# Kernel optimization log

Measured on AMD Instinct MI355X. Metric: run time of the kernel, lower is better.

## Reference

```python
import jax, jax.numpy as jnp
import numpy as np

B, S, D, H = 4, 2048, 1024, 16
DH = D // H
LN_EPS = 1e-5


def setup_inputs() -> dict:
    key = jax.random.key(0)
    ks = jax.random.split(key, 8)
    q = jax.random.normal(ks[0], (B, S, D), dtype=jnp.float32)
    k = jax.random.normal(ks[1], (B, S, D), dtype=jnp.float32)
    v = jax.random.normal(ks[2], (B, S, D), dtype=jnp.float32)
    masks = jax.random.randint(ks[3], (B, S, S), 0, 2, dtype=jnp.int32)
    proj_Q = jax.random.normal(ks[4], (D,), dtype=jnp.float32)
    proj_K = jax.random.normal(ks[5], (D,), dtype=jnp.float32)
    proj_V = jax.random.normal(ks[6], (D,), dtype=jnp.float32)
    gamma = jnp.ones((D,), dtype=jnp.float32)
    beta = jnp.zeros((D,), dtype=jnp.float32)
    return {"q": q, "k": k, "v": v, "masks": masks,
            "proj_Q": proj_Q, "proj_K": proj_K, "proj_V": proj_V,
            "gamma": gamma, "beta": beta}


def _split_heads(x):
    # x: [B,S,D] -> permute(0,2,1) -> [B,D,S] -> view(B*H, DH, S) -> permute -> [B*H, S, DH]
    xt = jnp.transpose(x, (0, 2, 1))              # [B,D,S]
    xt = xt.reshape(B * H, DH, S)                 # [B*H,DH,S] (batch-major head split)
    return jnp.transpose(xt, (0, 2, 1))           # [B*H,S,DH]


def reference(q, k, v, masks, proj_Q, proj_K, proj_V, gamma, beta):
    # Source bug preserved: projections all applied to `x` == q; k, v are ignored.
    x = q
    Qh = _split_heads(x * proj_Q)                 # [B*H,S,DH]
    Kh = _split_heads(x * proj_K)
    Vh = _split_heads(x * proj_V)

    # masks cat'd along dim 0 num_head times (head-major tiling, as in source)
    m = jnp.tile(masks, (H, 1, 1)).astype(bool)   # [H*B,S,S]

    scores = jnp.einsum('nqd,nkd->nqk', Qh, Kh) / jnp.sqrt(jnp.float32(D))
    scores = jnp.where(m, jnp.float32(-1e-10), scores)  # source uses -1e-10, not -inf
    attn = jax.nn.softmax(scores, axis=2)
    ctx = jnp.einsum('nqk,nkd->nqd', attn, Vh)    # [B*H,S,DH]

    # merge heads back: [B*H,S,DH] -> [B*H,DH,S] -> [B,D,S] -> [B,S,D]
    ctx = jnp.transpose(ctx, (0, 2, 1)).reshape(B, D, S)
    ctx = jnp.transpose(ctx, (0, 2, 1))

    out = ctx + q                                  # dropout(p=0) is identity
    mu = jnp.mean(out, axis=-1, keepdims=True)
    var = jnp.var(out, axis=-1, keepdims=True)
    out = (out - mu) * jax.lax.rsqrt(var + LN_EPS) * gamma + beta
    return out
```

## Files before the change

### kernel.cpp

```cpp
#include <hip/hip_runtime.h>
#include <math.h>

#define Bn 4
#define Sn 2048
#define Dn 1024
#define Hn 16
#define DHn 64
#define QT 128
#define KT 64
#define STR 72

typedef __attribute__((ext_vector_type(8))) short short8;
typedef __attribute__((ext_vector_type(4))) float f32x4;

__device__ __forceinline__ ushort f2bf(float f) {
    union { float f; unsigned u; } x; x.f = f;
    unsigned r = x.u + 0x7fffu + ((x.u >> 16) & 1u);
    return (ushort)(r >> 16);
}

__device__ __forceinline__ unsigned pack_bf2(float lo, float hi) {
    unsigned r;
    asm("v_cvt_pk_bf16_f32 %0, %1, %2" : "=v"(r) : "v"(lo), "v"(hi));
    return r;
}

__device__ __forceinline__ float fexp2(float x) { return __builtin_amdgcn_exp2f(x); }

__global__ __launch_bounds__(256)
void prep_kv3(const float* __restrict__ xin, const float* __restrict__ pK,
              const float* __restrict__ pV, ushort* __restrict__ Kw,
              ushort* __restrict__ Vw)
{
    __shared__ ushort LK[64 * STR];
    __shared__ ushort LV[64 * STR];
    const int kt = blockIdx.x, n = blockIdx.y, b = n >> 4, h = n & 15;
    const int t = threadIdx.x;
    const int sl = t >> 2, dq = (t & 3) * 16;

    const float* xp  = xin + ((size_t)b * Sn + kt * 64 + sl) * Dn + h * DHn + dq;
    const float* pkp = pK + h * DHn + dq;
    const float* pvp = pV + h * DHn + dq;

    float xv[16], pk[16], pv[16];
    #pragma unroll
    for (int j = 0; j < 4; ++j) {
        float4 a  = ((const float4*)xp)[j];
        float4 kk = ((const float4*)pkp)[j];
        float4 vv = ((const float4*)pvp)[j];
        xv[4*j+0] = a.x;  xv[4*j+1] = a.y;  xv[4*j+2] = a.z;  xv[4*j+3] = a.w;
        pk[4*j+0] = kk.x; pk[4*j+1] = kk.y; pk[4*j+2] = kk.z; pk[4*j+3] = kk.w;
        pv[4*j+0] = vv.x; pv[4*j+1] = vv.y; pv[4*j+2] = vv.z; pv[4*j+3] = vv.w;
    }
    unsigned kw[8], vw[8];
    #pragma unroll
    for (int j = 0; j < 8; ++j) {
        kw[j] = pack_bf2(xv[2*j] * pk[2*j], xv[2*j+1] * pk[2*j+1]);
        vw[j] = pack_bf2(xv[2*j] * pv[2*j], xv[2*j+1] * pv[2*j+1]);
    }
    *(uint4*)&LK[sl * STR + dq]     = make_uint4(kw[0], kw[1], kw[2], kw[3]);
    *(uint4*)&LK[sl * STR + dq + 8] = make_uint4(kw[4], kw[5], kw[6], kw[7]);
    *(uint4*)&LV[sl * STR + dq]     = make_uint4(vw[0], vw[1], vw[2], vw[3]);
    *(uint4*)&LV[sl * STR + dq + 8] = make_uint4(vw[4], vw[5], vw[6], vw[7]);
    __syncthreads();

    ushort* kout = Kw + ((size_t)n * 32 + kt) * 4096;
    ushort* vout = Vw + ((size_t)n * 32 + kt) * 4096;
    #pragma unroll
    for (int i = 0; i < 2; ++i) {
        int c  = t * 2 + i;
        int f  = c >> 6, lc = c & 63;
        int key = (f >> 1) * 16 + (lc & 15);
        int dh0 = (f & 1) * 32 + (lc >> 4) * 8;
        *(uint4*)(kout + c * 8) = *(const uint4*)&LK[key * STR + dh0];
        int dg = f & 3, hh = f >> 2;
        int dhv = dg * 16 + (lc & 15);
        ushort tmp[8];
        #pragma unroll
        for (int e = 0; e < 8; ++e) {
            int p  = hh * 32 + (lc >> 4) * 8 + e;
            int ss = (p & 32) | ((p & 4) << 2) | ((p & 24) >> 1) | (p & 3);
            tmp[e] = LV[ss * STR + dhv];
        }
        unsigned o0 = (unsigned)tmp[0] | ((unsigned)tmp[1] << 16);
        unsigned o1 = (unsigned)tmp[2] | ((unsigned)tmp[3] << 16);
        unsigned o2 = (unsigned)tmp[4] | ((unsigned)tmp[5] << 16);
        unsigned o3 = (unsigned)tmp[6] | ((unsigned)tmp[7] << 16);
        *(uint4*)(vout + c * 8) = make_uint4(o0, o1, o2, o3);
    }
}

__global__ __launch_bounds__(256)
void mask_pack(const int* __restrict__ masks, unsigned long long* __restrict__ mpack)
{
    const int t = threadIdx.x, l = t & 63;
    const int wid_g = (blockIdx.x * 256 + t) >> 6;
    #pragma unroll 4
    for (int i = 0; i < 16; ++i) {
        int word = wid_g * 16 + i;
        int row  = word >> 5, wd = word & 31;
        int m = masks[(size_t)row * 2048 + wd * 64 + l];
        unsigned long long bits = __ballot(m != 0);
        if (l == 0) mpack[word] = bits;
    }
}

__global__ __launch_bounds__(256, 2)
void attn_fast3(const float* __restrict__ xin, const unsigned long long* __restrict__ mpack,
                const float* __restrict__ pQ, const ushort* __restrict__ Kw,
                const ushort* __restrict__ Vw, float* __restrict__ out)
{
    __shared__ __attribute__((aligned(16))) ushort S[16384];

    const int id   = blockIdx.x;
    const int xcd  = id & 7, pos = id >> 3;
    const int n    = (pos >> 4) * 8 + xcd;
    const int q0   = (pos & 15) * 128;
    const int b    = n >> 4;
    const int h    = n & 15;
    const int mb   = n & 3;

    const int t  = threadIdx.x;
    const int w  = t >> 6;
    const int l  = t & 63;
    const int G  = l >> 4;
    const int li = l & 15;
    const int G4 = G * 4;

    const float C2 = 0.0450842200277800f;
    const float* xb = xin + (size_t)b * Sn * Dn + h * DHn;
    const float pq_s = pQ[h * DHn + l] * C2;
    #pragma unroll
    for (int i = 0; i < 8; ++i) {
        #pragma unroll
        for (int j = 0; j < 4; ++j) {
            int qr = i * 4 + j;
            float v = xb[(size_t)(q0 + w * 32 + qr) * Dn + l];
            S[(w * 32 + qr) * STR + l] = f2bf(v * pq_s);
        }
    }
    short8 qf[2][2];
    #pragma unroll
    for (int qs = 0; qs < 2; ++qs)
        #pragma unroll
        for (int kk = 0; kk < 2; ++kk)
            qf[qs][kk] = *(const short8*)&S[(w*32 + qs*16 + li) * STR + kk*32 + G*8];
    __syncthreads();

    const f32x4 Z4 = {0.f, 0.f, 0.f, 0.f};
    const short8 VONES = {(short)0x3F80, (short)0x3F80, (short)0x3F80, (short)0x3F80,
                          (short)0x3F80, (short)0x3F80, (short)0x3F80, (short)0x3F80};

    f32x4 acc_o[2][4];
    f32x4 acc_l[2];
    #pragma unroll
    for (int qs = 0; qs < 2; ++qs) {
        #pragma unroll
        for (int dg = 0; dg < 4; ++dg) acc_o[qs][dg] = (f32x4){0.f, 0.f, 0.f, 0.f};
        acc_l[qs] = (f32x4){0.f, 0.f, 0.f, 0.f};
    }

    const ushort* kwf = Kw + (size_t)n * 131072 + (w * 2) * 512 + (size_t)l * 8;
    const ushort* vwf = Vw + (size_t)n * 131072 + (w * 2) * 512 + (size_t)l * 8;
    const int fo0 = (w * 2) * 512 + l * 8;
    const int fo1 = (w * 2 + 1) * 512 + l * 8;

    const int row0 = q0 + w * 32 + li;
    const unsigned long long* mrow0 = mpack + (size_t)(mb * 2048 + row0) * 32;
    const unsigned long long* mrow1 = mpack + (size_t)(mb * 2048 + row0 + 16) * 32;

    unsigned long long mA0, mA1, mB0, mB1;

    {
        short8 a = *(const short8*)kwf;
        short8 c = *(const short8*)(kwf + 512);
        short8 d = *(const short8*)vwf;
        short8 e = *(const short8*)(vwf + 512);
        mA0 = mrow0[0]; mA1 = mrow1[0];
        *(short8*)&S[fo0] = a;
        *(short8*)&S[fo1] = c;
        *(short8*)&S[8192 + fo0] = d;
        *(short8*)&S[8192 + fo1] = e;
    }

#define BODY(CUR, NXT, MC0, MC1, MN0, MN1, KTv, PF)                                   \
    {                                                                                  \
        __syncthreads();                     \
               \
        f32x4 s_[2][4];                                                                \
        __builtin_amdgcn_s_setprio(1);                                                 \
        _Pragma("unroll")                                                              \
        for (int kg = 0; kg < 4; ++kg) {                                               \
            short8 kf0 = *(const short8*)&S[(CUR)*4096 + (kg*2+0)*512 + l*8];          \
            short8 kf1 = *(const short8*)&S[(CUR)*4096 + (kg*2+1)*512 + l*8];          \
            s_[0][kg] = __builtin_amdgcn_mfma_f32_16x16x32_bf16(kf0, qf[0][0], Z4, 0, 0, 0); \
            s_[1][kg] = __builtin_amdgcn_mfma_f32_16x16x32_bf16(kf0, qf[1][0], Z4, 0, 0, 0); \
            s_[0][kg] = __builtin_amdgcn_mfma_f32_16x16x32_bf16(kf1, qf[0][1], s_[0][kg], 0, 0, 0); \
            s_[1][kg] = __builtin_amdgcn_mfma_f32_16x16x32_bf16(kf1, qf[1][1], s_[1][kg], 0, 0, 0); \
        }                                                                              \
        __builtin_amdgcn_s_setprio(0);                                                 \
                        \
        short8 kst0, kst1, vst0, vst1;                                                 \
        if (PF) {                                                                      \
            const ushort* kp = kwf + (size_t)((KTv)+1) * 4096;                         \
            const ushort* vp = vwf + (size_t)((KTv)+1) * 4096;                         \
            kst0 = *(const short8*)kp;  kst1 = *(const short8*)(kp + 512);             \
            vst0 = *(const short8*)vp;  vst1 = *(const short8*)(vp + 512);             \
            MN0 = mrow0[(KTv)+1];       MN1 = mrow1[(KTv)+1];                          \
        }                                                                              \
                         \
        short8 pf[2][2];                                                               \
        _Pragma("unroll")                                                              \
        for (int qs = 0; qs < 2; ++qs) {                                               \
            unsigned mlo = (unsigned)(qs ? (MC1) : (MC0));                             \
            unsigned mhi = (unsigned)((qs ? (MC1) : (MC0)) >> 32);                     \
            float ev[16];                                                              \
            _Pragma("unroll")                                                          \
            for (int kg = 0; kg < 4; ++kg) {                                           \
                unsigned dw  = (kg < 2) ? mlo : mhi;                                   \
                unsigned nib = (dw >> ((kg & 1) * 16 + G4)) & 15u;                     \
                _Pragma("unroll")                                                      \
                for (int r = 0; r < 4; ++r) {                                          \
                    float tt = (nib & (1u << r)) ? 0.f : s_[qs][kg][r];                \
                    ev[kg*4 + r] = fexp2(tt);                                          \
                }                                                                      \
            }                                                                          \
            _Pragma("unroll")                                                          \
            for (int hh = 0; hh < 2; ++hh) {                                           \
                union { unsigned u[4]; short8 v; } pu;                                 \
                pu.u[0] = pack_bf2(ev[hh*8+0], ev[hh*8+1]);                            \
                pu.u[1] = pack_bf2(ev[hh*8+2], ev[hh*8+3]);                            \
                pu.u[2] = pack_bf2(ev[hh*8+4], ev[hh*8+5]);                            \
                pu.u[3] = pack_bf2(ev[hh*8+6], ev[hh*8+7]);                            \
                pf[qs][hh] = pu.v;                                                     \
            }                                                                          \
        }                                                                              \
                                                \
        __builtin_amdgcn_s_setprio(1);                                                 \
        _Pragma("unroll")                                                              \
        for (int hh = 0; hh < 2; ++hh) {                                               \
            short8 vf0 = *(const short8*)&S[8192 + (CUR)*4096 + (hh*4+0)*512 + l*8];   \
            short8 vf1 = *(const short8*)&S[8192 + (CUR)*4096 + (hh*4+1)*512 + l*8];   \
            short8 vf2 = *(const short8*)&S[8192 + (CUR)*4096 + (hh*4+2)*512 + l*8];   \
            short8 vf3 = *(const short8*)&S[8192 + (CUR)*4096 + (hh*4+3)*512 + l*8];   \
            _Pragma("unroll")                                                          \
            for (int qs = 0; qs < 2; ++qs) {                                           \
                acc_o[qs][0] = __builtin_amdgcn_mfma_f32_16x16x32_bf16(pf[qs][hh], vf0, acc_o[qs][0], 0, 0, 0); \
                acc_o[qs][1] = __builtin_amdgcn_mfma_f32_16x16x32_bf16(pf[qs][hh], vf1, acc_o[qs][1], 0, 0, 0); \
                acc_o[qs][2] = __builtin_amdgcn_mfma_f32_16x16x32_bf16(pf[qs][hh], vf2, acc_o[qs][2], 0, 0, 0); \
                acc_o[qs][3] = __builtin_amdgcn_mfma_f32_16x16x32_bf16(pf[qs][hh], vf3, acc_o[qs][3], 0, 0, 0); \
                acc_l[qs]    = __builtin_amdgcn_mfma_f32_16x16x32_bf16(pf[qs][hh], VONES, acc_l[qs], 0, 0, 0); \
            }                                                                          \
        }                                                                              \
        __builtin_amdgcn_s_setprio(0);                                                 \
        \
        if (PF) {                                                                      \
            *(short8*)&S[(NXT)*4096 + fo0] = kst0;                                     \
            *(short8*)&S[(NXT)*4096 + fo1] = kst1;                                     \
            *(short8*)&S[8192 + (NXT)*4096 + fo0] = vst0;                              \
            *(short8*)&S[8192 + (NXT)*4096 + fo1] = vst1;                              \
        }                                                                              \
    }

    for (int kt = 0; kt < 32; kt += 2) {
        BODY(0, 1, mA0, mA1, mB0, mB1, kt, true)
        BODY(1, 0, mB0, mB1, mA0, mA1, kt + 1, (kt + 1 < 31))
    }
#undef BODY

    #pragma unroll
    for (int qs = 0; qs < 2; ++qs) {
        #pragma unroll
        for (int r = 0; r < 4; ++r) {
            float inv = 1.f / acc_l[qs][r];
            int qg = q0 + w*32 + qs*16 + G4 + r;
            float* ob = out + ((size_t)b * Sn + qg) * Dn + h * DHn;
            #pragma unroll
            for (int dg = 0; dg < 4; ++dg)
                ob[dg*16 + li] = acc_o[qs][dg][r] * inv;
        }
    }
}

__global__ __launch_bounds__(256)
void prep_kv(const float* __restrict__ xin, const float* __restrict__ pK,
             const float* __restrict__ pV, ushort* __restrict__ Kbf,
             ushort* __restrict__ Vtw)
{
    __shared__ ushort Ls[64 * STR];
    const int n = blockIdx.y, b = n >> 4, h = n & 15;
    const int s0 = blockIdx.x * 64;
    const int t = threadIdx.x;
    const int sl = t >> 2, dq = (t & 3) * 16;

    const float* xp = xin + (size_t)b * Sn * Dn + (size_t)(s0 + sl) * Dn + h * DHn + dq;
    const float* pkp = pK + h * DHn + dq;
    const float* pvp = pV + h * DHn + dq;

    float xv[16], pk[16], pv[16];
    #pragma unroll
    for (int j = 0; j < 4; ++j) {
        float4 a = ((const float4*)xp)[j];
        float4 kk = ((const float4*)pkp)[j];
        float4 vv = ((const float4*)pvp)[j];
        xv[4*j+0] = a.x;  xv[4*j+1] = a.y;  xv[4*j+2] = a.z;  xv[4*j+3] = a.w;
        pk[4*j+0] = kk.x; pk[4*j+1] = kk.y; pk[4*j+2] = kk.z; pk[4*j+3] = kk.w;
        pv[4*j+0] = vv.x; pv[4*j+1] = vv.y; pv[4*j+2] = vv.z; pv[4*j+3] = vv.w;
    }
    unsigned kw[8], vw[8];
    #pragma unroll
    for (int j = 0; j < 8; ++j) {
        kw[j] = pack_bf2(xv[2*j] * pk[2*j], xv[2*j+1] * pk[2*j+1]);
        vw[j] = pack_bf2(xv[2*j] * pv[2*j], xv[2*j+1] * pv[2*j+1]);
    }
    ushort* kdst = Kbf + ((size_t)n * Sn + s0 + sl) * DHn + dq;
    *(uint4*)kdst       = make_uint4(kw[0], kw[1], kw[2], kw[3]);
    *(uint4*)(kdst + 8) = make_uint4(kw[4], kw[5], kw[6], kw[7]);

    *(uint4*)&Ls[sl * STR + dq]     = make_uint4(vw[0], vw[1], vw[2], vw[3]);
    *(uint4*)&Ls[sl * STR + dq + 8] = make_uint4(vw[4], vw[5], vw[6], vw[7]);
    __syncthreads();

    const int dh = t >> 2, p4 = t & 3;
    ushort ov[16];
    #pragma unroll
    for (int j = 0; j < 16; ++j) {
        int p  = p4 * 16 + j;
        int ss = (p & 32) | ((p & 4) << 2) | ((p & 24) >> 1) | (p & 3);
        ov[j] = Ls[ss * STR + dh];
    }
    unsigned ow[8];
    #pragma unroll
    for (int j = 0; j < 8; ++j) ow[j] = (unsigned)ov[2*j] | ((unsigned)ov[2*j+1] << 16);
    ushort* vdst = Vtw + ((size_t)n * DHn + dh) * Sn + s0 + p4 * 16;
    *(uint4*)vdst       = make_uint4(ow[0], ow[1], ow[2], ow[3]);
    *(uint4*)(vdst + 8) = make_uint4(ow[4], ow[5], ow[6], ow[7]);
}

__global__ __launch_bounds__(256, 4)
void attn_fast2(const float* __restrict__ xin, const int* __restrict__ masks,
                const float* __restrict__ pQ, const ushort* __restrict__ Kbf,
                const ushort* __restrict__ Vtw, float* __restrict__ out)
{
    __shared__ ushort Ks[KT * STR];
    __shared__ ushort Vts[DHn * STR];

    const int n  = blockIdx.y;
    const int b  = n >> 4;
    const int h  = n & 15;
    const int mb = n & 3;
    const int q0 = blockIdx.x * QT;

    const int t  = threadIdx.x;
    const int w  = t >> 6;
    const int l  = t & 63;
    const int G  = l >> 4;
    const int li = l & 15;

    const float C2 = 0.0450842200277800f;
    const float* xb = xin + (size_t)b * Sn * Dn + h * DHn;
    const float pq_s = pQ[h * DHn + l] * C2;
    ushort* qstage = ((w < 2) ? Ks : Vts) + (w & 1) * (32 * STR);
    #pragma unroll
    for (int i = 0; i < 8; ++i) {
        #pragma unroll
        for (int j = 0; j < 4; ++j) {
            int qr = i * 4 + j;
            float v = xb[(size_t)(q0 + w * 32 + qr) * Dn + l];
            qstage[qr * STR + l] = f2bf(v * pq_s);
        }
    }
    short8 qf[2][2];
    #pragma unroll
    for (int qs = 0; qs < 2; ++qs)
        #pragma unroll
        for (int kk = 0; kk < 2; ++kk)
            qf[qs][kk] = *(const short8*)&qstage[(qs*16 + li) * STR + kk*32 + G*8];

    f32x4 acc_o[2][4];
    float lsum[2];
    #pragma unroll
    for (int qs = 0; qs < 2; ++qs) {
        #pragma unroll
        for (int dg = 0; dg < 4; ++dg) acc_o[qs][dg] = (f32x4){0.f, 0.f, 0.f, 0.f};
        lsum[qs] = 0.f;
    }

    const int* mq = masks + (size_t)mb * Sn * Sn + (size_t)(q0 + w*32 + li) * Sn;

    const int srow = w * 16 + (l >> 2);
    const int part = (l & 3) * 16;
    const ushort* ksrc = Kbf + (size_t)n * Sn * DHn + (size_t)srow * DHn + part;
    const ushort* vsrc = Vtw + (size_t)n * DHn * Sn + (size_t)srow * Sn + part;
    ushort* kdst = &Ks[srow * STR + part];
    ushort* vdst = &Vts[srow * STR + part];

    for (int kt = 0; kt < Sn / KT; ++kt) {
        __syncthreads();
        const ushort* kp = ksrc + (size_t)kt * KT * DHn;
        const ushort* vp = vsrc + kt * KT;
        short8 k0 = *(const short8*)kp, k1 = *(const short8*)(kp + 8);
        short8 v0 = *(const short8*)vp, v1 = *(const short8*)(vp + 8);
        *(short8*)kdst       = k0;
        *(short8*)(kdst + 8) = k1;
        *(short8*)vdst       = v0;
        *(short8*)(vdst + 8) = v1;
        __syncthreads();

        f32x4 s[2][4];
        #pragma unroll
        for (int qs = 0; qs < 2; ++qs)
            #pragma unroll
            for (int kg = 0; kg < 4; ++kg) s[qs][kg] = (f32x4){0.f, 0.f, 0.f, 0.f};
        __builtin_amdgcn_s_setprio(1);
        #pragma unroll
        for (int kg = 0; kg < 4; ++kg) {
            #pragma unroll
            for (int kk = 0; kk < 2; ++kk) {
                short8 kf = *(const short8*)&Ks[(kg*16 + li) * STR + kk*32 + G*8];
                s[0][kg] = __builtin_amdgcn_mfma_f32_16x16x32_bf16(kf, qf[0][kk], s[0][kg], 0, 0, 0);
                s[1][kg] = __builtin_amdgcn_mfma_f32_16x16x32_bf16(kf, qf[1][kk], s[1][kg], 0, 0, 0);
            }
        }
        __builtin_amdgcn_s_setprio(0);

        short8 pf[2][2];
        #pragma unroll
        for (int qs = 0; qs < 2; ++qs) {
            int4 mv[4];
            #pragma unroll
            for (int kg = 0; kg < 4; ++kg)
                mv[kg] = *(const int4*)(mq + (size_t)qs*16*Sn + kt*KT + kg*16 + G*4);
            float ev[16];
            #pragma unroll
            for (int kg = 0; kg < 4; ++kg) {
                int ma[4] = {mv[kg].x, mv[kg].y, mv[kg].z, mv[kg].w};
                #pragma unroll
                for (int r = 0; r < 4; ++r) {
                    float tt = ma[r] ? 0.f : s[qs][kg][r];
                    ev[kg*4 + r] = fexp2(tt);
                }
            }
            lsum[qs] += (((ev[0]+ev[1])+(ev[2]+ev[3])) + ((ev[4]+ev[5])+(ev[6]+ev[7])))
                      + (((ev[8]+ev[9])+(ev[10]+ev[11])) + ((ev[12]+ev[13])+(ev[14]+ev[15])));
            #pragma unroll
            for (int hh = 0; hh < 2; ++hh) {
                union { unsigned u[4]; short8 v; } pu;
                pu.u[0] = pack_bf2(ev[hh*8+0], ev[hh*8+1]);
                pu.u[1] = pack_bf2(ev[hh*8+2], ev[hh*8+3]);
                pu.u[2] = pack_bf2(ev[hh*8+4], ev[hh*8+5]);
                pu.u[3] = pack_bf2(ev[hh*8+6], ev[hh*8+7]);
                pf[qs][hh] = pu.v;
            }
        }

        #pragma unroll
        for (int hh = 0; hh < 2; ++hh) {
            short8 vf[4];
            #pragma unroll
            for (int dg = 0; dg < 4; ++dg)
                vf[dg] = *(const short8*)&Vts[(dg*16 + li) * STR + hh*32 + G*8];
            __builtin_amdgcn_s_setprio(1);
            #pragma unroll
            for (int qs = 0; qs < 2; ++qs)
                #pragma unroll
                for (int dg = 0; dg < 4; ++dg)
                    acc_o[qs][dg] = __builtin_amdgcn_mfma_f32_16x16x32_bf16(pf[qs][hh], vf[dg], acc_o[qs][dg], 0, 0, 0);
            __builtin_amdgcn_s_setprio(0);
        }
    }

    #pragma unroll
    for (int qs = 0; qs < 2; ++qs) {
        float v = lsum[qs];
        v += __shfl_xor(v, 16, 64);
        v += __shfl_xor(v, 32, 64);
        lsum[qs] = v;
    }

    #pragma unroll
    for (int qs = 0; qs < 2; ++qs) {
        #pragma unroll
        for (int r = 0; r < 4; ++r) {
            float lv = __shfl(lsum[qs], (l & 48) | (G * 4 + r), 64);
            float inv = 1.f / lv;
            int qg = q0 + w*32 + qs*16 + G*4 + r;
            float* ob = out + ((size_t)b * Sn + qg) * Dn + h * DHn;
            #pragma unroll
            for (int dg = 0; dg < 4; ++dg)
                ob[dg*16 + li] = acc_o[qs][dg][r] * inv;
        }
    }
}

__global__ __launch_bounds__(256)
void ln_kernel(const float* __restrict__ qin, const float* __restrict__ gamma,
               const float* __restrict__ beta, float* __restrict__ out)
{
    const int row = blockIdx.x;
    const int t   = threadIdx.x;
    const size_t base = (size_t)row * Dn + t * 4;

    float4 c = *(const float4*)(out + base);
    float4 r = *(const float4*)(qin + base);
    float4 v = make_float4(c.x + r.x, c.y + r.y, c.z + r.z, c.w + r.w);

    float sum = v.x + v.y + v.z + v.w;
    float sq  = v.x * v.x + v.y * v.y + v.z * v.z + v.w * v.w;
    #pragma unroll
    for (int off = 32; off >= 1; off >>= 1) {
        sum += __shfl_xor(sum, off, 64);
        sq  += __shfl_xor(sq,  off, 64);
    }
    __shared__ float as_[4], aq_[4];
    const int wid = t >> 6, ln = t & 63;
    if (ln == 0) { as_[wid] = sum; aq_[wid] = sq; }
    __syncthreads();
    sum = as_[0] + as_[1] + as_[2] + as_[3];
    sq  = aq_[0] + aq_[1] + aq_[2] + aq_[3];

    const float mean = sum * (1.f / Dn);
    const float var  = sq * (1.f / Dn) - mean * mean;
    const float rstd = rsqrtf(var + 1e-5f);

    float4 ga = *(const float4*)(gamma + t * 4);
    float4 be = *(const float4*)(beta + t * 4);
    float4 o;
    o.x = (v.x - mean) * rstd * ga.x + be.x;
    o.y = (v.y - mean) * rstd * ga.y + be.y;
    o.z = (v.z - mean) * rstd * ga.z + be.z;
    o.w = (v.w - mean) * rstd * ga.w + be.w;
    *(float4*)(out + base) = o;
}

extern "C" void kernel_launch(void* const* d_in, const int* in_sizes, int n_in,
                              void* d_out, int out_size, void* d_ws, size_t ws_size,
                              hipStream_t stream) {
    const float* q     = (const float*)d_in[0];
    const int*   masks = (const int*)d_in[3];
    const float* pQ    = (const float*)d_in[4];
    const float* pK    = (const float*)d_in[5];
    const float* pV    = (const float*)d_in[6];
    const float* gamma = (const float*)d_in[7];
    const float* beta  = (const float*)d_in[8];
    float* out = (float*)d_out;
    (void)in_sizes; (void)n_in; (void)out_size;

    const size_t elems = (size_t)Bn * Hn * Sn * DHn;
    const size_t kvbytes = elems * 2 * sizeof(ushort);
    const size_t need3 = kvbytes + (size_t)4 * Sn * 32 * 8;

    if (ws_size >= need3) {
        ushort* Kw = (ushort*)d_ws;
        ushort* Vw = Kw + elems;
        unsigned long long* mpack = (unsigned long long*)((char*)d_ws + kvbytes);
        prep_kv3<<<dim3(32, 64), 256, 0, stream>>>(q, pK, pV, Kw, Vw);
        mask_pack<<<4096, 256, 0, stream>>>(masks, mpack);
        attn_fast3<<<1024, 256, 0, stream>>>(q, mpack, pQ, Kw, Vw, out);
    } else if (ws_size >= kvbytes) {
        ushort* Kbf = (ushort*)d_ws;
        ushort* Vtw = Kbf + elems;
        prep_kv<<<dim3(Sn / 64, Bn * Hn), 256, 0, stream>>>(q, pK, pV, Kbf, Vtw);
        attn_fast2<<<dim3(Sn / QT, Bn * Hn), 256, 0, stream>>>(q, masks, pQ, Kbf, Vtw, out);
    }
    ln_kernel<<<Bn * Sn, 256, 0, stream>>>(q, gamma, beta, out);
}
```

Baseline: 140.4 us.

## Fuse KV prep with mask packing, tighten mask select asm, raise occupancy hint

The K/V prep kernel and the mask bit-packing kernel are merged into one launch, with blocks past 2048 doing mask packing, which removes a kernel launch and lets the two memory-bound phases overlap. Inside the attention loop, the nibble extraction and masked-score select are rewritten with v_bfe/v_bfi inline asm instead of compiler-generated shifts and selects. The attention kernel's launch bounds go from 2 to 3 blocks per CU, which caps registers and may cause spills.

New measurement: 137.9 us. About the same (-1.8%).

```diff
diff --git a/kernel.cpp b/kernel.cpp
--- a/kernel.cpp
+++ b/kernel.cpp
@@ -27,15 +27,38 @@
 
 __device__ __forceinline__ float fexp2(float x) { return __builtin_amdgcn_exp2f(x); }
 
+__device__ __forceinline__ float mask_sel(unsigned nib, int r, float s) {
+    int sx; unsigned tb;
+    asm("v_bfe_i32 %0, %1, %2, 1" : "=v"(sx) : "v"(nib), "i"(r));
+    asm("v_bfi_b32 %0, %1, 0, %2" : "=v"(tb) : "v"(sx), "v"(__float_as_uint(s)));
+    return __uint_as_float(tb);
+}
+
 __global__ __launch_bounds__(256)
-void prep_kv3(const float* __restrict__ xin, const float* __restrict__ pK,
-              const float* __restrict__ pV, ushort* __restrict__ Kw,
-              ushort* __restrict__ Vw)
+void prep_fused(const float* __restrict__ xin, const float* __restrict__ pK,
+                const float* __restrict__ pV, const int* __restrict__ masks,
+                ushort* __restrict__ Kw, ushort* __restrict__ Vw,
+                unsigned long long* __restrict__ mpack)
 {
     __shared__ ushort LK[64 * STR];
     __shared__ ushort LV[64 * STR];
-    const int kt = blockIdx.x, n = blockIdx.y, b = n >> 4, h = n & 15;
     const int t = threadIdx.x;
+
+    if (blockIdx.x >= 2048) {
+        const int l = t & 63;
+        const int wid_g = ((blockIdx.x - 2048) * 256 + t) >> 6;
+        #pragma unroll 4
+        for (int i = 0; i < 16; ++i) {
+            int word = wid_g * 16 + i;
+            int row  = word >> 5, wd = word & 31;
+            int m = masks[(size_t)row * 2048 + wd * 64 + l];
+            unsigned long long bits = __ballot(m != 0);
+            if (l == 0) mpack[word] = bits;
+        }
+        return;
+    }
+
+    const int kt = blockIdx.x & 31, n = blockIdx.x >> 5, b = n >> 4, h = n & 15;
     const int sl = t >> 2, dq = (t & 3) * 16;
 
     const float* xp  = xin + ((size_t)b * Sn + kt * 64 + sl) * Dn + h * DHn + dq;
@@ -90,22 +113,7 @@
     }
 }
 
-__global__ __launch_bounds__(256)
-void mask_pack(const int* __restrict__ masks, unsigned long long* __restrict__ mpack)
-{
-    const int t = threadIdx.x, l = t & 63;
-    const int wid_g = (blockIdx.x * 256 + t) >> 6;
-    #pragma unroll 4
-    for (int i = 0; i < 16; ++i) {
-        int word = wid_g * 16 + i;
-        int row  = word >> 5, wd = word & 31;
-        int m = masks[(size_t)row * 2048 + wd * 64 + l];
-        unsigned long long bits = __ballot(m != 0);
-        if (l == 0) mpack[word] = bits;
-    }
-}
-
-__global__ __launch_bounds__(256, 2)
+__global__ __launch_bounds__(256, 3)
 void attn_fast3(const float* __restrict__ xin, const unsigned long long* __restrict__ mpack,
                 const float* __restrict__ pQ, const ushort* __restrict__ Kw,
                 const ushort* __restrict__ Vw, float* __restrict__ out)
@@ -126,6 +134,7 @@
     const int G  = l >> 4;
     const int li = l & 15;
     const int G4 = G * 4;
+    const int G4p16 = G4 + 16;
 
     const float C2 = 0.0450842200277800f;
     const float* xb = xin + (size_t)b * Sn * Dn + h * DHn;
@@ -208,7 +217,7 @@
             vst0 = *(const short8*)vp;  vst1 = *(const short8*)(vp + 512);             \
             MN0 = mrow0[(KTv)+1];       MN1 = mrow1[(KTv)+1];                          \
         }                                                                              \
-                         \
+                       \
         short8 pf[2][2];                                                               \
         _Pragma("unroll")                                                              \
         for (int qs = 0; qs < 2; ++qs) {                                               \
@@ -217,13 +226,13 @@
             float ev[16];                                                              \
             _Pragma("unroll")                                                          \
             for (int kg = 0; kg < 4; ++kg) {                                           \
-                unsigned dw  = (kg < 2) ? mlo : mhi;                                   \
-                unsigned nib = (dw >> ((kg & 1) * 16 + G4)) & 15u;                     \
+                unsigned dwh = (kg < 2) ? mlo : mhi;                                   \
+                unsigned nib;                                                          \
+                asm("v_bfe_u32 %0, %1, %2, 4" : "=v"(nib)                              \
+                    : "v"(dwh), "v"((kg & 1) ? G4p16 : G4));                           \
                 _Pragma("unroll")                                                      \
-                for (int r = 0; r < 4; ++r) {                                          \
-                    float tt = (nib & (1u << r)) ? 0.f : s_[qs][kg][r];                \
-                    ev[kg*4 + r] = fexp2(tt);                                          \
-                }                                                                      \
+                for (int r = 0; r < 4; ++r)                                            \
+                    ev[kg*4 + r] = fexp2(mask_sel(nib, r, s_[qs][kg][r]));             \
             }                                                                          \
             _Pragma("unroll")                                                          \
             for (int hh = 0; hh < 2; ++hh) {                                           \
@@ -253,7 +262,7 @@
             }                                                                          \
         }                                                                              \
         __builtin_amdgcn_s_setprio(0);                                                 \
-        \
+                                     \
         if (PF) {                                                                      \
             *(short8*)&S[(NXT)*4096 + fo0] = kst0;                                     \
             *(short8*)&S[(NXT)*4096 + fo1] = kst1;                                     \
@@ -554,8 +563,7 @@
         ushort* Kw = (ushort*)d_ws;
         ushort* Vw = Kw + elems;
         unsigned long long* mpack = (unsigned long long*)((char*)d_ws + kvbytes);
-        prep_kv3<<<dim3(32, 64), 256, 0, stream>>>(q, pK, pV, Kw, Vw);
-        mask_pack<<<4096, 256, 0, stream>>>(masks, mpack);
+        prep_fused<<<6144, 256, 0, stream>>>(q, pK, pV, masks, Kw, Vw, mpack);
         attn_fast3<<<1024, 256, 0, stream>>>(q, mpack, pQ, Kw, Vw, out);
     } else if (ws_size >= kvbytes) {
         ushort* Kbf = (ushort*)d_ws;
```
